# Performance work log

Measured on AMD Instinct MI355X. Metric: run time of the kernel, lower is better.

The kernel has to match this reference:

```python
import jax, jax.numpy as jnp
import numpy as np

RANK, N, T, S = 8, 64, 64, 64
IN_F, OUT_F = N * T, N * S  # 4096, 4096


def setup_inputs() -> dict:
    key = jax.random.key(0)
    k1, k2, k3, k4 = jax.random.split(key, 4)
    scale = 1.0 / np.sqrt(IN_F)
    x = jax.random.normal(k1, (8, 2048, IN_F), dtype=jnp.float32)
    A = jax.random.normal(k2, (RANK, N, T), dtype=jnp.float32) * scale
    B = jax.random.normal(k3, (RANK, S, N), dtype=jnp.float32) * scale
    bias = jax.random.uniform(k4, (OUT_F,), dtype=jnp.float32, minval=-scale, maxval=scale)
    return {"x": x, "A": A, "B": B, "bias": bias}


def reference(x, A, B, bias):
    # Kronecker-product weight reconstruction: sum over rank b of
    # W[i*S+k, j*N+m] = sum_b A[b,i,j] * B[b,k,m]
    W = jnp.einsum('bij,bkm->ikjm', A, B).reshape(OUT_F, IN_F)
    # F.linear: x @ W.T + bias
    return jnp.einsum('bsi,oi->bso', x, W) + bias
```

## Files before the change

### kernel.cpp

```cpp
#include <hip/hip_runtime.h>
#include <stdint.h>

#define M_DIM 16384
#define N_DIM 4096
#define K_DIM 4096
#define KTILES (K_DIM / 32)

typedef short short8 __attribute__((ext_vector_type(8)));
typedef unsigned short ushort8 __attribute__((ext_vector_type(8)));
typedef float f32x4 __attribute__((ext_vector_type(4)));

__device__ __forceinline__ unsigned short f2b(float f) {
    union { float f; uint32_t u; } v; v.f = f;
    return (unsigned short)((v.u + 0x7FFFu + ((v.u >> 16) & 1u)) >> 16);
}

__device__ __forceinline__ void async_ld16(const void* g, void* l) {
    __builtin_amdgcn_global_load_lds(
        (const __attribute__((address_space(1))) uint32_t*)g,
        (__attribute__((address_space(3))) uint32_t*)l, 16, 0, 0);
}

#define VMCNT(n) asm volatile("s_waitcnt vmcnt(" #n ")" ::: "memory")
#define LGKM0    asm volatile("s_waitcnt lgkmcnt(0)" ::: "memory")

__global__ __launch_bounds__(256) void build_w_kernel(
    const float* __restrict__ A, const float* __restrict__ B,
    unsigned short* __restrict__ W)
{
    size_t idx = ((size_t)blockIdx.x * 256 + threadIdx.x) * 8;
    int o = (int)(idx >> 12);
    int c = (int)(idx & 4095);
    int i = o >> 6, k = o & 63;
    int j = c >> 6, m0 = c & 63;

    float acc[8];
#pragma unroll
    for (int t = 0; t < 8; ++t) acc[t] = 0.0f;
#pragma unroll
    for (int b = 0; b < 8; ++b) {
        float a = A[b * 4096 + i * 64 + j];
        const float4* bp = (const float4*)&B[b * 4096 + k * 64 + m0];
        float4 b0 = bp[0], b1 = bp[1];
        acc[0] += a * b0.x; acc[1] += a * b0.y;
        acc[2] += a * b0.z; acc[3] += a * b0.w;
        acc[4] += a * b1.x; acc[5] += a * b1.y;
        acc[6] += a * b1.z; acc[7] += a * b1.w;
    }
    ushort8 r;
#pragma unroll
    for (int t = 0; t < 8; ++t) r[t] = f2b(acc[t]);
    *(ushort8*)&W[idx] = r;
}

__global__ __launch_bounds__(256) void cvt_x_kernel(
    const float* __restrict__ x, unsigned short* __restrict__ xb)
{
    size_t idx = ((size_t)blockIdx.x * 256 + threadIdx.x) * 8;
    const float4* gp = (const float4*)&x[idx];
    float4 v0 = gp[0], v1 = gp[1];
    ushort8 r;
    r[0] = f2b(v0.x); r[1] = f2b(v0.y); r[2] = f2b(v0.z); r[3] = f2b(v0.w);
    r[4] = f2b(v1.x); r[5] = f2b(v1.y); r[6] = f2b(v1.z); r[7] = f2b(v1.w);
    *(ushort8*)&xb[idx] = r;
}

__global__ __launch_bounds__(512, 2) void gemm256_kernel(
    const unsigned short* __restrict__ xb,
    const unsigned short* __restrict__ W,
    const float* __restrict__ bias,
    float* __restrict__ out)
{
    __shared__ __align__(16) unsigned short AsB[4][256 * 32];
    __shared__ __align__(16) unsigned short BsB[4][256 * 32];

    const int tid = threadIdx.x;
    const int wave = tid >> 6;
    const int lane = tid & 63;
    const int quad = lane >> 4;
    const int l15 = lane & 15;
    const int wr = wave >> 2;
    const int wc = wave & 3;

    const int wg = ((blockIdx.x & 7) << 7) | (blockIdx.x >> 3);
    const size_t mbase = (size_t)(wg >> 4) * 256;
    const int nbase = (wg & 15) * 256;

    const int arow0 = wr * 128 + l15;
    const int brow0 = wc * 64 + l15;

    f32x4 acc[8][4];
#pragma unroll
    for (int a = 0; a < 8; ++a)
#pragma unroll
        for (int b = 0; b < 4; ++b)
            acc[a][b] = (f32x4){0.0f, 0.0f, 0.0f, 0.0f};

    auto stage_half = [&](int tile, int li) {
        const int slot = tile & 3;
        const int f = li * 512 + tid;
        const int row = f >> 2;
        const int kof = tile * 32 + ((((f & 3) ^ ((row >> 1) & 3))) << 3);
        unsigned short* ab = &AsB[slot][(li * 512 + wave * 64) * 8];
        unsigned short* bb = &BsB[slot][(li * 512 + wave * 64) * 8];
        async_ld16(&xb[(mbase + row) * K_DIM + kof], ab);
        async_ld16(&W[(size_t)(nbase + row) * K_DIM + kof], bb);
    };
    auto frag = [&](const unsigned short* buf, int row) -> short8 {
        return *(const short8*)&buf[row * 32 + ((quad ^ ((row >> 1) & 3)) << 3)];
    };

    stage_half(0, 0); stage_half(0, 1);
    stage_half(1, 0); stage_half(1, 1);
    stage_half(2, 0); stage_half(2, 1);
    VMCNT(8);
    __builtin_amdgcn_s_barrier();

#pragma unroll 1
    for (int t = 0; t < KTILES; ++t) {
        const unsigned short* As_c = AsB[t & 3];
        const unsigned short* Bs_c = BsB[t & 3];
        const bool pf = (t + 3) < KTILES;

        short8 af[4], bf[4];
#pragma unroll
        for (int mt = 0; mt < 4; ++mt) af[mt] = frag(As_c, arow0 + mt * 16);
#pragma unroll
        for (int nt = 0; nt < 4; ++nt) bf[nt] = frag(Bs_c, brow0 + nt * 16);
        if (pf) stage_half(t + 3, 0);
        __builtin_amdgcn_s_barrier();
        LGKM0;
        __builtin_amdgcn_sched_barrier(0);
        __builtin_amdgcn_s_setprio(1);
#pragma unroll
        for (int mt = 0; mt < 4; ++mt)
#pragma unroll
            for (int nt = 0; nt < 4; ++nt)
                acc[mt][nt] = __builtin_amdgcn_mfma_f32_16x16x32_bf16(
                    af[mt], bf[nt], acc[mt][nt], 0, 0, 0);
        __builtin_amdgcn_s_setprio(0);
        __builtin_amdgcn_s_barrier();

        short8 ag[4];
#pragma unroll
        for (int mt = 0; mt < 4; ++mt) ag[mt] = frag(As_c, arow0 + 64 + mt * 16);
        if (pf) stage_half(t + 3, 1);
        __builtin_amdgcn_s_barrier();
        LGKM0;
        __builtin_amdgcn_sched_barrier(0);
        __builtin_amdgcn_s_setprio(1);
#pragma unroll
        for (int mt = 0; mt < 4; ++mt)
#pragma unroll
            for (int nt = 0; nt < 4; ++nt)
                acc[4 + mt][nt] = __builtin_amdgcn_mfma_f32_16x16x32_bf16(
                    ag[mt], bf[nt], acc[4 + mt][nt], 0, 0, 0);
        __builtin_amdgcn_s_setprio(0);
        if (t < KTILES - 3)       { VMCNT(8); }
        else if (t == KTILES - 3) { VMCNT(4); }
        else                      { VMCNT(0); }
        __builtin_amdgcn_s_barrier();
    }

    float bv[4];
#pragma unroll
    for (int nt = 0; nt < 4; ++nt) bv[nt] = bias[nbase + wc * 64 + nt * 16 + l15];
#pragma unroll
    for (int mt = 0; mt < 8; ++mt) {
#pragma unroll
        for (int r = 0; r < 4; ++r) {
            const size_t row = mbase + wr * 128 + mt * 16 + quad * 4 + r;
            float* orow = out + row * N_DIM + nbase + wc * 64 + l15;
#pragma unroll
            for (int nt = 0; nt < 4; ++nt)
                orow[nt * 16] = acc[mt][nt][r] + bv[nt];
        }
    }
}

__global__ __launch_bounds__(256, 2) void gemm128_f32(
    const float* __restrict__ xf,
    const unsigned short* __restrict__ W,
    const float* __restrict__ bias,
    float* __restrict__ out)
{
    __shared__ unsigned short As[128 * 32];
    __shared__ unsigned short Bs[128 * 32];

    const int tid = threadIdx.x;
    const int wave = tid >> 6;
    const int lane = tid & 63;
    const int quad = lane >> 4;
    const int l15 = lane & 15;
    const int wm = (wave >> 1) * 64;
    const int wn = (wave & 1) * 64;
    const size_t mbase = (size_t)blockIdx.y * 128;
    const int nbase = blockIdx.x * 128;

    f32x4 acc[4][4];
#pragma unroll
    for (int a = 0; a < 4; ++a)
#pragma unroll
        for (int b = 0; b < 4; ++b)
            acc[a][b] = (f32x4){0.0f, 0.0f, 0.0f, 0.0f};

    for (int k0 = 0; k0 < K_DIM; k0 += 32) {
        {
            const int issue0 = wave * 2;
#pragma unroll
            for (int t = 0; t < 2; ++t) {
                const int isn = issue0 + t;
                const int row = isn * 16 + (lane >> 2);
                const int kc = (lane & 3) * 8;
                async_ld16(&W[(size_t)(nbase + row) * K_DIM + k0 + kc],
                           &Bs[isn * 512]);
            }
        }
        {
            const int row = tid >> 1;
            const int half = tid & 1;
            const float* gp = xf + (mbase + row) * K_DIM + k0 + half * 16;
            float4 v0 = ((const float4*)gp)[0];
            float4 v1 = ((const float4*)gp)[1];
            float4 v2 = ((const float4*)gp)[2];
            float4 v3 = ((const float4*)gp)[3];
            ushort8 lo, hi;
            lo[0] = f2b(v0.x); lo[1] = f2b(v0.y); lo[2] = f2b(v0.z); lo[3] = f2b(v0.w);
            lo[4] = f2b(v1.x); lo[5] = f2b(v1.y); lo[6] = f2b(v1.z); lo[7] = f2b(v1.w);
            hi[0] = f2b(v2.x); hi[1] = f2b(v2.y); hi[2] = f2b(v2.z); hi[3] = f2b(v2.w);
            hi[4] = f2b(v3.x); hi[5] = f2b(v3.y); hi[6] = f2b(v3.z); hi[7] = f2b(v3.w);
            *(ushort8*)&As[row * 32 + half * 16] = lo;
            *(ushort8*)&As[row * 32 + half * 16 + 8] = hi;
        }
        __syncthreads();

        short8 af[4], bf[4];
#pragma unroll
        for (int mt = 0; mt < 4; ++mt)
            af[mt] = *(const short8*)&As[(wm + mt * 16 + l15) * 32 + quad * 8];
#pragma unroll
        for (int nt = 0; nt < 4; ++nt)
            bf[nt] = *(const short8*)&Bs[(wn + nt * 16 + l15) * 32 + quad * 8];
#pragma unroll
        for (int mt = 0; mt < 4; ++mt)
#pragma unroll
            for (int nt = 0; nt < 4; ++nt)
                acc[mt][nt] = __builtin_amdgcn_mfma_f32_16x16x32_bf16(
                    af[mt], bf[nt], acc[mt][nt], 0, 0, 0);
        __syncthreads();
    }

    float bv[4];
#pragma unroll
    for (int nt = 0; nt < 4; ++nt) bv[nt] = bias[nbase + wn + nt * 16 + l15];
#pragma unroll
    for (int mt = 0; mt < 4; ++mt) {
#pragma unroll
        for (int r = 0; r < 4; ++r) {
            const size_t row = mbase + wm + mt * 16 + quad * 4 + r;
            float* orow = out + row * N_DIM + nbase + wn + l15;
#pragma unroll
            for (int nt = 0; nt < 4; ++nt)
                orow[nt * 16] = acc[mt][nt][r] + bv[nt];
        }
    }
}

extern "C" void kernel_launch(void* const* d_in, const int* in_sizes, int n_in,
                              void* d_out, int out_size, void* d_ws, size_t ws_size,
                              hipStream_t stream)
{
    const float* x = (const float*)d_in[0];
    const float* A = (const float*)d_in[1];
    const float* B = (const float*)d_in[2];
    const float* bias = (const float*)d_in[3];
    float* out = (float*)d_out;

    unsigned short* Wb = (unsigned short*)d_ws;
    const size_t wbytes = (size_t)N_DIM * K_DIM * 2;
    const size_t xbytes = (size_t)M_DIM * K_DIM * 2;

    build_w_kernel<<<(N_DIM * (size_t)K_DIM) / 8 / 256, 256, 0, stream>>>(A, B, Wb);

    if (ws_size >= wbytes + xbytes) {
        unsigned short* xbuf = (unsigned short*)((char*)d_ws + wbytes);
        cvt_x_kernel<<<((size_t)M_DIM * K_DIM) / 8 / 256, 256, 0, stream>>>(x, xbuf);
        gemm256_kernel<<<dim3(1024), 512, 0, stream>>>(xbuf, Wb, bias, out);
    } else {
        gemm128_f32<<<dim3(N_DIM / 128, M_DIM / 128), 256, 0, stream>>>(x, Wb, bias, out);
    }
}
```

Before: 1.050 ms.

## Merge W build and x conversion into one launch; single-barrier GEMM main loop

The separate W-reconstruction and x-to-bf16 kernels are merged into one prep kernel that picks its role from the block index, removing a launch and the gap between the two. In the GEMM main loop, all A/B fragments for a k-tile are now read up front and both prefetch halves are issued together. That removes two of the three barriers per iteration and the explicit lgkmcnt waits. Correctness now relies on the 4-slot ring depth and the final barrier to keep a slot from being overwritten while another wave still reads it. Holding more fragments live raises register pressure.

```diff
diff --git a/kernel.cpp b/kernel.cpp
--- a/kernel.cpp
+++ b/kernel.cpp
@@ -22,13 +22,13 @@
 }
 
 #define VMCNT(n) asm volatile("s_waitcnt vmcnt(" #n ")" ::: "memory")
-#define LGKM0    asm volatile("s_waitcnt lgkmcnt(0)" ::: "memory")
-
-__global__ __launch_bounds__(256) void build_w_kernel(
+
+__device__ __forceinline__ void build_w_body(
+    int bid, int tid,
     const float* __restrict__ A, const float* __restrict__ B,
     unsigned short* __restrict__ W)
 {
-    size_t idx = ((size_t)blockIdx.x * 256 + threadIdx.x) * 8;
+    size_t idx = ((size_t)bid * 256 + tid) * 8;
     int o = (int)(idx >> 12);
     int c = (int)(idx & 4095);
     int i = o >> 6, k = o & 63;
@@ -53,16 +53,30 @@
     *(ushort8*)&W[idx] = r;
 }
 
-__global__ __launch_bounds__(256) void cvt_x_kernel(
-    const float* __restrict__ x, unsigned short* __restrict__ xb)
-{
-    size_t idx = ((size_t)blockIdx.x * 256 + threadIdx.x) * 8;
-    const float4* gp = (const float4*)&x[idx];
-    float4 v0 = gp[0], v1 = gp[1];
-    ushort8 r;
-    r[0] = f2b(v0.x); r[1] = f2b(v0.y); r[2] = f2b(v0.z); r[3] = f2b(v0.w);
-    r[4] = f2b(v1.x); r[5] = f2b(v1.y); r[6] = f2b(v1.z); r[7] = f2b(v1.w);
-    *(ushort8*)&xb[idx] = r;
+__global__ __launch_bounds__(256) void build_w_kernel(
+    const float* __restrict__ A, const float* __restrict__ B,
+    unsigned short* __restrict__ W)
+{
+    build_w_body(blockIdx.x, threadIdx.x, A, B, W);
+}
+
+__global__ __launch_bounds__(256) void prep_kernel(
+    const float* __restrict__ x, unsigned short* __restrict__ xb,
+    const float* __restrict__ A, const float* __restrict__ B,
+    unsigned short* __restrict__ W)
+{
+    int bid = blockIdx.x;
+    if (bid < 32768) {
+        size_t idx = ((size_t)bid * 256 + threadIdx.x) * 8;
+        const float4* gp = (const float4*)&x[idx];
+        float4 v0 = gp[0], v1 = gp[1];
+        ushort8 r;
+        r[0] = f2b(v0.x); r[1] = f2b(v0.y); r[2] = f2b(v0.z); r[3] = f2b(v0.w);
+        r[4] = f2b(v1.x); r[5] = f2b(v1.y); r[6] = f2b(v1.z); r[7] = f2b(v1.w);
+        *(ushort8*)&xb[idx] = r;
+    } else {
+        build_w_body(bid - 32768, threadIdx.x, A, B, W);
+    }
 }
 
 __global__ __launch_bounds__(512, 2) void gemm256_kernel(
@@ -115,22 +129,25 @@
     stage_half(2, 0); stage_half(2, 1);
     VMCNT(8);
     __builtin_amdgcn_s_barrier();
+    __builtin_amdgcn_sched_barrier(0);
 
 #pragma unroll 1
     for (int t = 0; t < KTILES; ++t) {
         const unsigned short* As_c = AsB[t & 3];
         const unsigned short* Bs_c = BsB[t & 3];
-        const bool pf = (t + 3) < KTILES;
-
-        short8 af[4], bf[4];
+
+        short8 af[4], bf[4], ag[4];
 #pragma unroll
         for (int mt = 0; mt < 4; ++mt) af[mt] = frag(As_c, arow0 + mt * 16);
 #pragma unroll
         for (int nt = 0; nt < 4; ++nt) bf[nt] = frag(Bs_c, brow0 + nt * 16);
-        if (pf) stage_half(t + 3, 0);
-        __builtin_amdgcn_s_barrier();
-        LGKM0;
-        __builtin_amdgcn_sched_barrier(0);
+#pragma unroll
+        for (int mt = 0; mt < 4; ++mt) ag[mt] = frag(As_c, arow0 + 64 + mt * 16);
+        if ((t + 3) < KTILES) {
+            stage_half(t + 3, 0);
+            stage_half(t + 3, 1);
+        }
+
         __builtin_amdgcn_s_setprio(1);
 #pragma unroll
         for (int mt = 0; mt < 4; ++mt)
@@ -138,17 +155,6 @@
             for (int nt = 0; nt < 4; ++nt)
                 acc[mt][nt] = __builtin_amdgcn_mfma_f32_16x16x32_bf16(
                     af[mt], bf[nt], acc[mt][nt], 0, 0, 0);
-        __builtin_amdgcn_s_setprio(0);
-        __builtin_amdgcn_s_barrier();
-
-        short8 ag[4];
-#pragma unroll
-        for (int mt = 0; mt < 4; ++mt) ag[mt] = frag(As_c, arow0 + 64 + mt * 16);
-        if (pf) stage_half(t + 3, 1);
-        __builtin_amdgcn_s_barrier();
-        LGKM0;
-        __builtin_amdgcn_sched_barrier(0);
-        __builtin_amdgcn_s_setprio(1);
 #pragma unroll
         for (int mt = 0; mt < 4; ++mt)
 #pragma unroll
@@ -156,10 +162,13 @@
                 acc[4 + mt][nt] = __builtin_amdgcn_mfma_f32_16x16x32_bf16(
                     ag[mt], bf[nt], acc[4 + mt][nt], 0, 0, 0);
         __builtin_amdgcn_s_setprio(0);
+
+        __builtin_amdgcn_sched_barrier(0);
         if (t < KTILES - 3)       { VMCNT(8); }
         else if (t == KTILES - 3) { VMCNT(4); }
         else                      { VMCNT(0); }
         __builtin_amdgcn_s_barrier();
+        __builtin_amdgcn_sched_barrier(0);
     }
 
     float bv[4];
@@ -280,13 +289,12 @@
     const size_t wbytes = (size_t)N_DIM * K_DIM * 2;
     const size_t xbytes = (size_t)M_DIM * K_DIM * 2;
 
-    build_w_kernel<<<(N_DIM * (size_t)K_DIM) / 8 / 256, 256, 0, stream>>>(A, B, Wb);
-
     if (ws_size >= wbytes + xbytes) {
         unsigned short* xbuf = (unsigned short*)((char*)d_ws + wbytes);
-        cvt_x_kernel<<<((size_t)M_DIM * K_DIM) / 8 / 256, 256, 0, stream>>>(x, xbuf);
+        prep_kernel<<<32768 + 8192, 256, 0, stream>>>(x, xbuf, A, B, Wb);
         gemm256_kernel<<<dim3(1024), 512, 0, stream>>>(xbuf, Wb, bias, out);
     } else {
+        build_w_kernel<<<(N_DIM * (size_t)K_DIM) / 8 / 256, 256, 0, stream>>>(A, B, Wb);
         gemm128_f32<<<dim3(N_DIM / 128, M_DIM / 128), 256, 0, stream>>>(x, Wb, bias, out);
     }
 }
```

Result: faster. 951.3 us (-9.4%).
